# Kernel optimization log

Measured on AMD Instinct MI355X. Metric: run time of the kernel, lower is better.

Reference implementation:

```python
import jax, jax.numpy as jnp
import numpy as np

B, N, F = 16, 4096, 3

def setup_inputs() -> dict:
    key = jax.random.key(0)
    k1, k2 = jax.random.split(key)
    array1 = jax.random.normal(k1, (B, N, F), dtype=jnp.float32)
    array2 = jax.random.normal(k2, (B, N, F), dtype=jnp.float32)
    return {"array1": array1, "array2": array2}

def reference(array1, array2):
    # D[b, i, j] = ||array1[b, i] - array2[b, j]||^2, via expansion identity
    sq1 = jnp.sum(array1 * array1, axis=-1)              # [B, N1]
    sq2 = jnp.sum(array2 * array2, axis=-1)              # [B, N2]
    cross = jnp.einsum('bnd,bmd->bnm', array1, array2)   # [B, N1, N2]
    D = sq1[:, :, None] + sq2[:, None, :] - 2.0 * cross  # [B, N1, N2]
    # av_dist1: for each sample in array2, min dist to array1, then mean
    av_dist1 = jnp.mean(jnp.min(D, axis=1), axis=1)      # [B]
    # av_dist2: for each sample in array1, min dist to array2, then mean
    av_dist2 = jnp.mean(jnp.min(D, axis=2), axis=1)      # [B]
    dist = jnp.mean(0.5 * av_dist1 + 0.5 * av_dist2)
    return dist * 100.0
```

## Files before the change

kernel.cpp:

```cpp
#include <hip/hip_runtime.h>


constexpr int B_ = 16;
constexpr int N_ = 4096;
constexpr int BN = B_ * N_;
constexpr int BLK = 256;
constexpr int JSPLIT = 4;
constexpr int JCHUNK = N_ / JSPLIT;
constexpr int JT4 = JCHUNK / 16;

using bf16x8 = __attribute__((ext_vector_type(8))) __bf16;
using f32x4  = __attribute__((ext_vector_type(4))) float;

__device__ inline uint bf16_rne(float f) {
    uint u = __float_as_uint(f);
    return (u + 0x7FFFu + ((u >> 16) & 1u)) >> 16;
}
__device__ inline float bf16_f(uint h) { return __uint_as_float(h << 16); }

__global__ __launch_bounds__(BLK)
void prep_kernel(const float* __restrict__ a1, const float* __restrict__ a2,
                 uint4* __restrict__ A1, uint4* __restrict__ B1,
                 uint4* __restrict__ A2, uint4* __restrict__ B2) {
    int gi = blockIdx.x * BLK + threadIdx.x;
    const float* in = blockIdx.y ? a2 : a1;
    uint4* Ao = blockIdx.y ? A2 : A1;
    uint4* Bo = blockIdx.y ? B2 : B1;
    float x = in[3 * gi], y = in[3 * gi + 1], z = in[3 * gi + 2];
    float sq = fmaf(x, x, fmaf(y, y, z * z));
    float t = -0.5f * sq;
    uint hx = bf16_rne(x), hy = bf16_rne(y), hz = bf16_rne(z);
    uint lx = bf16_rne(x - bf16_f(hx));
    uint ly = bf16_rne(y - bf16_f(hy));
    uint lz = bf16_rne(z - bf16_f(hz));
    uint th = bf16_rne(t);
    uint tl = bf16_rne(t - bf16_f(th));
    const uint ONE = 0x3F80u;
    Ao[2 * gi]     = make_uint4(hx | (hy << 16), hz | (lx << 16), ly | (lz << 16), hx | (hy << 16));
    Ao[2 * gi + 1] = make_uint4(hz | (ONE << 16), ONE | (th << 16), tl, 0u);
    Bo[2 * gi]     = make_uint4(hx | (hy << 16), hz | (hx << 16), hy | (hz << 16), lx | (ly << 16));
    Bo[2 * gi + 1] = make_uint4(lz | (th << 16), tl | (ONE << 16), ONE, 0u);
}

#define FOLDP(Qa, Qb) {                                                          \
    f32x4 oA = __builtin_amdgcn_mfma_f32_16x16x32_bf16(a0, (Qa), cz, 0, 0, 0);   \
    f32x4 oB = __builtin_amdgcn_mfma_f32_16x16x32_bf16(a1, (Qa), cz, 0, 0, 0);   \
    f32x4 oC = __builtin_amdgcn_mfma_f32_16x16x32_bf16(a2, (Qa), cz, 0, 0, 0);   \
    f32x4 oD = __builtin_amdgcn_mfma_f32_16x16x32_bf16(a3, (Qa), cz, 0, 0, 0);   \
    f32x4 oE = __builtin_amdgcn_mfma_f32_16x16x32_bf16(a0, (Qb), cz, 0, 0, 0);   \
    f32x4 oF = __builtin_amdgcn_mfma_f32_16x16x32_bf16(a1, (Qb), cz, 0, 0, 0);   \
    f32x4 oG = __builtin_amdgcn_mfma_f32_16x16x32_bf16(a2, (Qb), cz, 0, 0, 0);   \
    f32x4 oH = __builtin_amdgcn_mfma_f32_16x16x32_bf16(a3, (Qb), cz, 0, 0, 0);   \
    _Pragma("unroll")                                                            \
    for (int r = 0; r < 4; ++r) {                                                \
        vm0[r] = fmaxf(fmaxf(vm0[r], oA[r]), oE[r]);                             \
        vm1[r] = fmaxf(fmaxf(vm1[r], oB[r]), oF[r]);                             \
        vm2[r] = fmaxf(fmaxf(vm2[r], oC[r]), oG[r]);                             \
        vm3[r] = fmaxf(fmaxf(vm3[r], oD[r]), oH[r]);                             \
    } }

__global__ __launch_bounds__(BLK, 4)
void minmax_kernel(const uint4* __restrict__ A1u, const uint4* __restrict__ B1u,
                   const uint4* __restrict__ A2u, const uint4* __restrict__ B2u,
                   float* __restrict__ vout) {
    __shared__ uint4 smem[JT4 * 32];
    int z = blockIdx.z, b = blockIdx.y;
    int d = z >> 2, s = z & 3;
    const bf16x8* __restrict__ Aarr = (const bf16x8*)(d ? A2u : A1u);
    const uint4*  __restrict__ Bu   = (d ? B1u : B2u);
    int tid = threadIdx.x;
    int L = tid & 63, w = tid >> 6;
    int lpt = L & 15;
    bool act = L < 32;
    int ibase = blockIdx.x * 256 + w * 64;
    int j0 = s * JCHUNK;

#pragma unroll
    for (int k = 0; k < 8; ++k) {
        int F = k * 256 + tid;
        int t = F >> 5, sl = F & 31;
        smem[F] = Bu[(size_t)(b * N_ + j0 + (t << 4) + (sl & 15)) * 2 + (sl >> 4)];
    }

    const bf16x8* pA = Aarr + (size_t)(b * N_ + ibase + lpt) * 2 + ((L >> 4) & 1);
    uint4 zu; zu.x = zu.y = zu.z = zu.w = 0u;
    bf16x8 zf = __builtin_bit_cast(bf16x8, zu);
    bf16x8 a0 = act ? pA[0] : zf;
    bf16x8 a1 = act ? pA[32] : zf;
    bf16x8 a2 = act ? pA[64] : zf;
    bf16x8 a3 = act ? pA[96] : zf;
    f32x4 cz = {0.f, 0.f, 0.f, 0.f};
    f32x4 vm0 = {-3.0e38f, -3.0e38f, -3.0e38f, -3.0e38f};
    f32x4 vm1 = vm0, vm2 = vm0, vm3 = vm0;

    __syncthreads();

    int lslot = L & 31;
#pragma unroll 2
    for (int t = 0; t < JT4; t += 2) {
        bf16x8 q0 = __builtin_bit_cast(bf16x8, smem[t * 32 + lslot]);
        bf16x8 q1 = __builtin_bit_cast(bf16x8, smem[t * 32 + 32 + lslot]);
        FOLDP(q0, q1)
    }

#pragma unroll
    for (int off = 1; off < 16; off <<= 1)
#pragma unroll
        for (int r = 0; r < 4; ++r) {
            vm0[r] = fmaxf(vm0[r], __shfl_xor(vm0[r], off));
            vm1[r] = fmaxf(vm1[r], __shfl_xor(vm1[r], off));
            vm2[r] = fmaxf(vm2[r], __shfl_xor(vm2[r], off));
            vm3[r] = fmaxf(vm3[r], __shfl_xor(vm3[r], off));
        }
    if (lpt == 0) {
        int rg = L >> 4;
#pragma unroll
        for (int r = 0; r < 4; ++r) {
            int row = rg * 4 + r;
            int o = z * BN + b * N_ + ibase + row;
            vout[o] = vm0[r];
            vout[o + 16] = vm1[r];
            vout[o + 32] = vm2[r];
            vout[o + 48] = vm3[r];
        }
    }
}

__device__ inline float block_sum_256(float v, float* red4) {
    for (int off = 32; off; off >>= 1) v += __shfl_down(v, off, 64);
    int lane = threadIdx.x & 63, w = threadIdx.x >> 6;
    if (lane == 0) red4[w] = v;
    __syncthreads();
    return red4[0] + red4[1] + red4[2] + red4[3];
}

__global__ __launch_bounds__(BLK)
void reduce1_kernel(const float* __restrict__ vout, float* __restrict__ sums) {
    int t = blockIdx.x * BLK + threadIdx.x;
    float m0 = fmaxf(fmaxf(vout[t], vout[BN + t]),
                     fmaxf(vout[2 * BN + t], vout[3 * BN + t]));
    float m1 = fmaxf(fmaxf(vout[4 * BN + t], vout[5 * BN + t]),
                     fmaxf(vout[6 * BN + t], vout[7 * BN + t]));
    float v = -2.0f * (m0 + m1);
    __shared__ float red4[4];
    float sm = block_sum_256(v, red4);
    if (threadIdx.x == 0) sums[blockIdx.x] = sm;
}

__global__ __launch_bounds__(BLK)
void reduce2_kernel(const float* __restrict__ sums, float* __restrict__ out) {
    float v = sums[threadIdx.x];
    __shared__ float red4[4];
    float sm = block_sum_256(v, red4);
    if (threadIdx.x == 0) out[0] = sm * (50.0f / (float)BN);
}

extern "C" void kernel_launch(void* const* d_in, const int* in_sizes, int n_in,
                              void* d_out, int out_size, void* d_ws, size_t ws_size,
                              hipStream_t stream) {
    const float* a1 = (const float*)d_in[0];
    const float* a2 = (const float*)d_in[1];
    char* ws = (char*)d_ws;
    uint4* A1 = (uint4*)(ws);
    uint4* B1 = (uint4*)(ws + (2u << 20));
    uint4* A2 = (uint4*)(ws + (4u << 20));
    uint4* B2 = (uint4*)(ws + (6u << 20));
    float* vout = (float*)(ws + (8u << 20));
    float* sums = (float*)(ws + (10u << 20));
    float* out = (float*)d_out;

    prep_kernel<<<dim3(BN / BLK, 2), BLK, 0, stream>>>(a1, a2, A1, B1, A2, B2);
    minmax_kernel<<<dim3(N_ / 256, B_, 2 * JSPLIT), BLK, 0, stream>>>(A1, B1, A2, B2, vout);
    reduce1_kernel<<<dim3(BN / BLK), BLK, 0, stream>>>(vout, sums);
    reduce2_kernel<<<dim3(1), BLK, 0, stream>>>(sums, out);
}
```

Before: 40.89 us.

## Compute both row and column minima from one distance pass instead of two

The old code ran the MFMA distance pass twice, once per direction, by swapping the roles of the two arrays. The new code computes only array1×array2 tiles and takes both the row max (per-i) and the column max (per-j) from the same MFMA outputs. Column partials are tree-reduced across the tile and written per i-chunk/wave into a large vcol buffer, then combined in reduce1. This halves MFMA work and the grid size, at the cost of extra VALU max and shuffle work in the inner loop, more global stores, and a 64-way strided reduction over about 16MB of partials.

After: 49.19 us. +20.3%, slower.

```diff
diff --git a/kernel.cpp b/kernel.cpp
--- a/kernel.cpp
+++ b/kernel.cpp
@@ -7,7 +7,7 @@
 constexpr int BLK = 256;
 constexpr int JSPLIT = 4;
 constexpr int JCHUNK = N_ / JSPLIT;
-constexpr int JT4 = JCHUNK / 16;
+constexpr int JT = JCHUNK / 16;
 
 using bf16x8 = __attribute__((ext_vector_type(8))) __bf16;
 using f32x4  = __attribute__((ext_vector_type(4))) float;
@@ -20,69 +20,64 @@
 
 __global__ __launch_bounds__(BLK)
 void prep_kernel(const float* __restrict__ a1, const float* __restrict__ a2,
-                 uint4* __restrict__ A1, uint4* __restrict__ B1,
-                 uint4* __restrict__ A2, uint4* __restrict__ B2) {
+                 uint4* __restrict__ A1, uint4* __restrict__ B2) {
     int gi = blockIdx.x * BLK + threadIdx.x;
-    const float* in = blockIdx.y ? a2 : a1;
-    uint4* Ao = blockIdx.y ? A2 : A1;
-    uint4* Bo = blockIdx.y ? B2 : B1;
-    float x = in[3 * gi], y = in[3 * gi + 1], z = in[3 * gi + 2];
-    float sq = fmaf(x, x, fmaf(y, y, z * z));
-    float t = -0.5f * sq;
-    uint hx = bf16_rne(x), hy = bf16_rne(y), hz = bf16_rne(z);
-    uint lx = bf16_rne(x - bf16_f(hx));
-    uint ly = bf16_rne(y - bf16_f(hy));
-    uint lz = bf16_rne(z - bf16_f(hz));
-    uint th = bf16_rne(t);
-    uint tl = bf16_rne(t - bf16_f(th));
     const uint ONE = 0x3F80u;
-    Ao[2 * gi]     = make_uint4(hx | (hy << 16), hz | (lx << 16), ly | (lz << 16), hx | (hy << 16));
-    Ao[2 * gi + 1] = make_uint4(hz | (ONE << 16), ONE | (th << 16), tl, 0u);
-    Bo[2 * gi]     = make_uint4(hx | (hy << 16), hz | (hx << 16), hy | (hz << 16), lx | (ly << 16));
-    Bo[2 * gi + 1] = make_uint4(lz | (th << 16), tl | (ONE << 16), ONE, 0u);
+    {
+        float x = a1[3 * gi], y = a1[3 * gi + 1], z = a1[3 * gi + 2];
+        float t = -0.5f * fmaf(x, x, fmaf(y, y, z * z));
+        uint hx = bf16_rne(x), hy = bf16_rne(y), hz = bf16_rne(z);
+        uint lx = bf16_rne(x - bf16_f(hx));
+        uint ly = bf16_rne(y - bf16_f(hy));
+        uint lz = bf16_rne(z - bf16_f(hz));
+        uint th = bf16_rne(t);
+        uint tl = bf16_rne(t - bf16_f(th));
+        A1[2 * gi]     = make_uint4(hx | (hy << 16), hz | (lx << 16),
+                                    ly | (lz << 16), hx | (hy << 16));
+        A1[2 * gi + 1] = make_uint4(hz | (ONE << 16), ONE | (th << 16), tl, 0u);
+    }
+    {
+        float x = a2[3 * gi], y = a2[3 * gi + 1], z = a2[3 * gi + 2];
+        float t = -0.5f * fmaf(x, x, fmaf(y, y, z * z));
+        uint hx = bf16_rne(x), hy = bf16_rne(y), hz = bf16_rne(z);
+        uint lx = bf16_rne(x - bf16_f(hx));
+        uint ly = bf16_rne(y - bf16_f(hy));
+        uint lz = bf16_rne(z - bf16_f(hz));
+        uint th = bf16_rne(t);
+        uint tl = bf16_rne(t - bf16_f(th));
+        B2[2 * gi]     = make_uint4(hx | (hy << 16), hz | (hx << 16),
+                                    hy | (hz << 16), lx | (ly << 16));
+        B2[2 * gi + 1] = make_uint4(lz | (th << 16), tl | (ONE << 16), ONE, 0u);
+    }
 }
 
-#define FOLDP(Qa, Qb) {                                                          \
-    f32x4 oA = __builtin_amdgcn_mfma_f32_16x16x32_bf16(a0, (Qa), cz, 0, 0, 0);   \
-    f32x4 oB = __builtin_amdgcn_mfma_f32_16x16x32_bf16(a1, (Qa), cz, 0, 0, 0);   \
-    f32x4 oC = __builtin_amdgcn_mfma_f32_16x16x32_bf16(a2, (Qa), cz, 0, 0, 0);   \
-    f32x4 oD = __builtin_amdgcn_mfma_f32_16x16x32_bf16(a3, (Qa), cz, 0, 0, 0);   \
-    f32x4 oE = __builtin_amdgcn_mfma_f32_16x16x32_bf16(a0, (Qb), cz, 0, 0, 0);   \
-    f32x4 oF = __builtin_amdgcn_mfma_f32_16x16x32_bf16(a1, (Qb), cz, 0, 0, 0);   \
-    f32x4 oG = __builtin_amdgcn_mfma_f32_16x16x32_bf16(a2, (Qb), cz, 0, 0, 0);   \
-    f32x4 oH = __builtin_amdgcn_mfma_f32_16x16x32_bf16(a3, (Qb), cz, 0, 0, 0);   \
-    _Pragma("unroll")                                                            \
-    for (int r = 0; r < 4; ++r) {                                                \
-        vm0[r] = fmaxf(fmaxf(vm0[r], oA[r]), oE[r]);                             \
-        vm1[r] = fmaxf(fmaxf(vm1[r], oB[r]), oF[r]);                             \
-        vm2[r] = fmaxf(fmaxf(vm2[r], oC[r]), oG[r]);                             \
-        vm3[r] = fmaxf(fmaxf(vm3[r], oD[r]), oH[r]);                             \
-    } }
+#define TREE16(o0, o1, o2, o3)                                                   \
+    fmaxf(fmaxf(fmaxf(fmaxf((o0)[0], (o0)[1]), fmaxf((o0)[2], (o0)[3])),         \
+                fmaxf(fmaxf((o1)[0], (o1)[1]), fmaxf((o1)[2], (o1)[3]))),        \
+          fmaxf(fmaxf(fmaxf((o2)[0], (o2)[1]), fmaxf((o2)[2], (o2)[3])),         \
+                fmaxf(fmaxf((o3)[0], (o3)[1]), fmaxf((o3)[2], (o3)[3]))))
 
 __global__ __launch_bounds__(BLK, 4)
-void minmax_kernel(const uint4* __restrict__ A1u, const uint4* __restrict__ B1u,
-                   const uint4* __restrict__ A2u, const uint4* __restrict__ B2u,
-                   float* __restrict__ vout) {
-    __shared__ uint4 smem[JT4 * 32];
-    int z = blockIdx.z, b = blockIdx.y;
-    int d = z >> 2, s = z & 3;
-    const bf16x8* __restrict__ Aarr = (const bf16x8*)(d ? A2u : A1u);
-    const uint4*  __restrict__ Bu   = (d ? B1u : B2u);
+void minmax_kernel(const uint4* __restrict__ A1u, const uint4* __restrict__ B2u,
+                   float* __restrict__ vrow, float* __restrict__ vcol) {
+    __shared__ uint4 smem[JT * 32];
+    int s = blockIdx.z, b = blockIdx.y, ic = blockIdx.x;
     int tid = threadIdx.x;
     int L = tid & 63, w = tid >> 6;
     int lpt = L & 15;
     bool act = L < 32;
-    int ibase = blockIdx.x * 256 + w * 64;
+    int ibase = ic * 256 + w * 64;
     int j0 = s * JCHUNK;
 
 #pragma unroll
     for (int k = 0; k < 8; ++k) {
         int F = k * 256 + tid;
         int t = F >> 5, sl = F & 31;
-        smem[F] = Bu[(size_t)(b * N_ + j0 + (t << 4) + (sl & 15)) * 2 + (sl >> 4)];
+        smem[F] = B2u[(size_t)(b * N_ + j0 + (t << 4) + (sl & 15)) * 2 + (sl >> 4)];
     }
 
-    const bf16x8* pA = Aarr + (size_t)(b * N_ + ibase + lpt) * 2 + ((L >> 4) & 1);
+    const bf16x8* pA = (const bf16x8*)A1u
+                     + (size_t)(b * N_ + ibase + lpt) * 2 + ((L >> 4) & 1);
     uint4 zu; zu.x = zu.y = zu.z = zu.w = 0u;
     bf16x8 zf = __builtin_bit_cast(bf16x8, zu);
     bf16x8 a0 = act ? pA[0] : zf;
@@ -96,11 +91,36 @@
     __syncthreads();
 
     int lslot = L & 31;
+    int cbase0 = (ic * 4 + w) * BN + b * N_ + j0 + lpt;
 #pragma unroll 2
-    for (int t = 0; t < JT4; t += 2) {
+    for (int t = 0; t < JT; t += 2) {
         bf16x8 q0 = __builtin_bit_cast(bf16x8, smem[t * 32 + lslot]);
         bf16x8 q1 = __builtin_bit_cast(bf16x8, smem[t * 32 + 32 + lslot]);
-        FOLDP(q0, q1)
+        f32x4 oA = __builtin_amdgcn_mfma_f32_16x16x32_bf16(a0, q0, cz, 0, 0, 0);
+        f32x4 oB = __builtin_amdgcn_mfma_f32_16x16x32_bf16(a1, q0, cz, 0, 0, 0);
+        f32x4 oC = __builtin_amdgcn_mfma_f32_16x16x32_bf16(a2, q0, cz, 0, 0, 0);
+        f32x4 oD = __builtin_amdgcn_mfma_f32_16x16x32_bf16(a3, q0, cz, 0, 0, 0);
+        f32x4 oE = __builtin_amdgcn_mfma_f32_16x16x32_bf16(a0, q1, cz, 0, 0, 0);
+        f32x4 oF = __builtin_amdgcn_mfma_f32_16x16x32_bf16(a1, q1, cz, 0, 0, 0);
+        f32x4 oG = __builtin_amdgcn_mfma_f32_16x16x32_bf16(a2, q1, cz, 0, 0, 0);
+        f32x4 oH = __builtin_amdgcn_mfma_f32_16x16x32_bf16(a3, q1, cz, 0, 0, 0);
+#pragma unroll
+        for (int r = 0; r < 4; ++r) {
+            vm0[r] = fmaxf(fmaxf(vm0[r], oA[r]), oE[r]);
+            vm1[r] = fmaxf(fmaxf(vm1[r], oB[r]), oF[r]);
+            vm2[r] = fmaxf(fmaxf(vm2[r], oC[r]), oG[r]);
+            vm3[r] = fmaxf(fmaxf(vm3[r], oD[r]), oH[r]);
+        }
+        float cA = TREE16(oA, oB, oC, oD);
+        float cB = TREE16(oE, oF, oG, oH);
+        cA = fmaxf(cA, __shfl_xor(cA, 16));
+        cA = fmaxf(cA, __shfl_xor(cA, 32));
+        cB = fmaxf(cB, __shfl_xor(cB, 16));
+        cB = fmaxf(cB, __shfl_xor(cB, 32));
+        if (L < 16) {
+            vcol[cbase0 + t * 16] = cA;
+            vcol[cbase0 + t * 16 + 16] = cB;
+        }
     }
 
 #pragma unroll
@@ -117,11 +137,11 @@
 #pragma unroll
         for (int r = 0; r < 4; ++r) {
             int row = rg * 4 + r;
-            int o = z * BN + b * N_ + ibase + row;
-            vout[o] = vm0[r];
-            vout[o + 16] = vm1[r];
-            vout[o + 32] = vm2[r];
-            vout[o + 48] = vm3[r];
+            int o = s * BN + b * N_ + ibase + row;
+            vrow[o] = vm0[r];
+            vrow[o + 16] = vm1[r];
+            vrow[o + 32] = vm2[r];
+            vrow[o + 48] = vm3[r];
         }
     }
 }
@@ -135,13 +155,16 @@
 }
 
 __global__ __launch_bounds__(BLK)
-void reduce1_kernel(const float* __restrict__ vout, float* __restrict__ sums) {
+void reduce1_kernel(const float* __restrict__ vrow, const float* __restrict__ vcol,
+                    float* __restrict__ sums) {
     int t = blockIdx.x * BLK + threadIdx.x;
-    float m0 = fmaxf(fmaxf(vout[t], vout[BN + t]),
-                     fmaxf(vout[2 * BN + t], vout[3 * BN + t]));
-    float m1 = fmaxf(fmaxf(vout[4 * BN + t], vout[5 * BN + t]),
-                     fmaxf(vout[6 * BN + t], vout[7 * BN + t]));
-    float v = -2.0f * (m0 + m1);
+    float rm = fmaxf(fmaxf(vrow[t], vrow[BN + t]),
+                     fmaxf(vrow[2 * BN + t], vrow[3 * BN + t]));
+    float cm = -3.0e38f;
+#pragma unroll
+    for (int ic = 0; ic < 64; ++ic)
+        cm = fmaxf(cm, vcol[(size_t)ic * BN + t]);
+    float v = rm + cm;
     __shared__ float red4[4];
     float sm = block_sum_256(v, red4);
     if (threadIdx.x == 0) sums[blockIdx.x] = sm;
@@ -152,7 +175,7 @@
     float v = sums[threadIdx.x];
     __shared__ float red4[4];
     float sm = block_sum_256(v, red4);
-    if (threadIdx.x == 0) out[0] = sm * (50.0f / (float)BN);
+    if (threadIdx.x == 0) out[0] = sm * (-100.0f / (float)BN);
 }
 
 extern "C" void kernel_launch(void* const* d_in, const int* in_sizes, int n_in,
@@ -162,15 +185,14 @@
     const float* a2 = (const float*)d_in[1];
     char* ws = (char*)d_ws;
     uint4* A1 = (uint4*)(ws);
-    uint4* B1 = (uint4*)(ws + (2u << 20));
-    uint4* A2 = (uint4*)(ws + (4u << 20));
-    uint4* B2 = (uint4*)(ws + (6u << 20));
-    float* vout = (float*)(ws + (8u << 20));
-    float* sums = (float*)(ws + (10u << 20));
+    uint4* B2 = (uint4*)(ws + (2u << 20));
+    float* vrow = (float*)(ws + (4u << 20));
+    float* vcol = (float*)(ws + (6u << 20));
+    float* sums = (float*)(ws + (23u << 20));
     float* out = (float*)d_out;
 
-    prep_kernel<<<dim3(BN / BLK, 2), BLK, 0, stream>>>(a1, a2, A1, B1, A2, B2);
-    minmax_kernel<<<dim3(N_ / 256, B_, 2 * JSPLIT), BLK, 0, stream>>>(A1, B1, A2, B2, vout);
-    reduce1_kernel<<<dim3(BN / BLK), BLK, 0, stream>>>(vout, sums);
+    prep_kernel<<<dim3(BN / BLK), BLK, 0, stream>>>(a1, a2, A1, B2);
+    minmax_kernel<<<dim3(N_ / 256, B_, JSPLIT), BLK, 0, stream>>>(A1, B2, vrow, vcol);
+    reduce1_kernel<<<dim3(BN / BLK), BLK, 0, stream>>>(vrow, vcol, sums);
     reduce2_kernel<<<dim3(1), BLK, 0, stream>>>(sums, out);
 }
```
